# Performance work log

Hardware: AMD Instinct MI355X
Metric: run time of the kernel (lower is better)

Reference implementation:

```python
import jax, jax.numpy as jnp
import numpy as np

B, L1, L2, H = 8, 384, 384, 128


def _lin(k, out_f, in_f, scale=0.05):
    kw, kb = jax.random.split(k)
    return (jax.random.normal(kw, (out_f, in_f), jnp.float32) * scale,
            jax.random.normal(kb, (out_f,), jnp.float32) * scale)


def setup_inputs() -> dict:
    key = jax.random.key(0)
    ks = jax.random.split(key, 10)
    Wq_w, Wq_b = _lin(ks[2], H, H)
    Wup_w, Wup_b = _lin(ks[3], H, H)
    Wvp_w, Wvp_b = _lin(ks[4], H, H)
    V_w, V_b = _lin(ks[5], 1, H)
    Wg_w, Wg_b = _lin(ks[6], 2 * H, 2 * H)
    W_ih, b_ih = _lin(ks[7], 4 * H, 2 * H)
    W_hh, b_hh = _lin(ks[8], 4 * H, H)
    return {
        "x": jax.random.normal(ks[0], (B, L1, H), jnp.float32),
        "x_mask": jnp.zeros((B, L1), dtype=bool),
        "y": jax.random.normal(ks[1], (B, L2, H), jnp.float32),
        "y_mask": jnp.zeros((B, L2), dtype=bool),
        "Wq_w": Wq_w, "Wq_b": Wq_b,
        "Wup_w": Wup_w, "Wup_b": Wup_b,
        "Wvp_w": Wvp_w, "Wvp_b": Wvp_b,
        "V_w": V_w, "V_b": V_b,
        "Wg_w": Wg_w, "Wg_b": Wg_b,
        "W_ih": W_ih, "W_hh": W_hh, "b_ih": b_ih, "b_hh": b_hh,
    }


def reference(x, x_mask, y, y_mask, Wq_w, Wq_b, Wup_w, Wup_b, Wvp_w, Wvp_b,
              V_w, V_b, Wg_w, Wg_b, W_ih, W_hh, b_ih, b_hh):
    b, l1, h = x.shape
    # projections (torch Linear: x @ W.T + b)
    x_proj = x @ Wup_w.T + Wup_b                      # [B, L1, H]
    y_proj = y @ Wq_w.T + Wq_b                        # [B, L2, H]
    # source feeds a constant zero hidden state into W_vp -> just its bias
    hidden_proj = jnp.zeros((h,), x.dtype) @ Wvp_w.T + Wvp_b  # [H]
    # additive attention scores: V . tanh(xp + yp + hp)
    sum_batch = jnp.tanh(x_proj[:, :, None, :] + y_proj[:, None, :, :] + hidden_proj)  # [B,L1,L2,H]
    s = jnp.einsum('btjh,h->btj', sum_batch, V_w[0]) + V_b[0]  # [B, L1, L2]
    # sum_mask = (1 - x_mask) outer (1 - y_mask)
    xm = 1.0 - x_mask.astype(s.dtype)
    ym = 1.0 - y_mask.astype(s.dtype)
    s = s * (xm[:, :, None] * ym[:, None, :])
    s = jnp.where(y_mask[:, None, :], -jnp.inf, s)
    alpha = jax.nn.softmax(s, axis=-1)                # [B, L1, L2]
    ct = jnp.einsum('btj,bjh->bth', alpha, y)         # [B, L1, H]
    merge = jnp.concatenate([x, ct], axis=2)          # [B, L1, 2H]
    gt = jax.nn.sigmoid(merge @ Wg_w.T + Wg_b)
    lstm_in = gt * merge                              # [B, L1, 2H]
    # single-layer unidirectional LSTM (torch gate order: i, f, g, o)
    gates_x = lstm_in @ W_ih.T + b_ih                 # [B, L1, 4H]

    def step(carry, gx):
        h_t, c_t = carry
        g = gx + h_t @ W_hh.T + b_hh
        i, f, gg, o = jnp.split(g, 4, axis=-1)
        c_n = jax.nn.sigmoid(f) * c_t + jax.nn.sigmoid(i) * jnp.tanh(gg)
        h_n = jax.nn.sigmoid(o) * jnp.tanh(c_n)
        return (h_n, c_n), h_n

    init = (jnp.zeros((b, h), x.dtype), jnp.zeros((b, h), x.dtype))
    _, hs = jax.lax.scan(step, init, jnp.swapaxes(gates_x, 0, 1))  # [L1, B, H]
    return jnp.swapaxes(hs, 0, 1)                     # [B, L1, H]
```

## Files before the change

### kernel.cpp

```cpp
#include <hip/hip_runtime.h>
#include <hip/hip_bf16.h>
#include <math.h>

typedef __attribute__((ext_vector_type(4))) float  float4v;
typedef __attribute__((ext_vector_type(2))) float  float2v;
typedef __attribute__((ext_vector_type(8))) short  short8;
typedef __attribute__((ext_vector_type(4))) int    int4v;

#define B_ 8
#define L_ 384
#define H_ 128

__device__ __forceinline__ float bflo(unsigned int u){ unsigned int t = u << 16; float f; __builtin_memcpy(&f,&t,4); return f; }
__device__ __forceinline__ unsigned short f2bf(float f){
  unsigned int t; __builtin_memcpy(&t,&f,4);
  return (unsigned short)((t + 0x7fffu + ((t>>16)&1u)) >> 16);
}
__device__ __forceinline__ float fsig(float x){ return __fdividef(1.f, 1.f + __expf(-x)); }

__device__ __forceinline__ void barrier_lds(){
  asm volatile("s_waitcnt lgkmcnt(0)\n\ts_barrier" ::: "memory");
}

template<int K>
__device__ __forceinline__ void mfma_rowgemm_body(
    unsigned short* in_s,
    const float* __restrict__ inA,
    const float* __restrict__ W, const float* __restrict__ bias,
    const float* __restrict__ bias2, float* __restrict__ out,
    int Ntotal, int act, int row0, int ob)
{
  constexpr int KP = K + 2;
  const int tid  = threadIdx.x;
  const int w    = tid >> 6;
  const int l    = tid & 63;
  const int c    = l & 15;
  const int quad = l >> 4;

  #pragma unroll
  for (int it = 0; it < K/32; ++it) {
    int idx = it*256 + tid;
    int r = idx / (K/4);
    int k = (idx % (K/4)) * 4;
    float4v f = *(const float4v*)(inA + (size_t)(row0+r)*K + k);
    unsigned int p0 = (unsigned int)f2bf(f.x) | ((unsigned int)f2bf(f.y) << 16);
    unsigned int p1 = (unsigned int)f2bf(f.z) | ((unsigned int)f2bf(f.w) << 16);
    *(unsigned int*)&in_s[r*KP + k]     = p0;
    *(unsigned int*)&in_s[r*KP + k + 2] = p1;
  }

  const int n = ob + w*16 + c;
  short8 bfr[K/32];
  #pragma unroll
  for (int kt = 0; kt < K/32; ++kt) {
    const float* src = W + (size_t)n*K + kt*32 + quad*8;
    float4v f0 = *(const float4v*)(src);
    float4v f1 = *(const float4v*)(src + 4);
    short8 v;
    v[0]=(short)f2bf(f0[0]); v[1]=(short)f2bf(f0[1]); v[2]=(short)f2bf(f0[2]); v[3]=(short)f2bf(f0[3]);
    v[4]=(short)f2bf(f1[0]); v[5]=(short)f2bf(f1[1]); v[6]=(short)f2bf(f1[2]); v[7]=(short)f2bf(f1[3]);
    bfr[kt] = v;
  }
  __syncthreads();

  const float4v z4 = {0.f,0.f,0.f,0.f};
  float4v acc0 = z4, acc1 = z4;
  #pragma unroll
  for (int kt = 0; kt < K/32; ++kt) {
    short8 a0 = *(const short8*)&in_s[(c     )*KP + kt*32 + quad*8];
    short8 a1 = *(const short8*)&in_s[(16 + c)*KP + kt*32 + quad*8];
    acc0 = __builtin_amdgcn_mfma_f32_16x16x32_bf16(a0, bfr[kt], acc0, 0,0,0);
    acc1 = __builtin_amdgcn_mfma_f32_16x16x32_bf16(a1, bfr[kt], acc1, 0,0,0);
  }

  const float C2 = 2.8853900817779268f;
  float bv = bias[n] + (bias2 ? bias2[n] : 0.f);
  #pragma unroll
  for (int mt = 0; mt < 2; ++mt) {
    float4v A = mt ? acc1 : acc0;
    #pragma unroll
    for (int r = 0; r < 4; ++r) {
      int m = mt*16 + quad*4 + r;
      float val = A[r] + bv;
      if (act == 4)
        val = __builtin_amdgcn_exp2f(C2 * val);
      if (act == 3)
        out[(size_t)(row0+m)*Ntotal + (n & 127)*4 + (n >> 7)] = val;
      else
        out[(size_t)(row0+m)*Ntotal + n] = val;
    }
  }
}

template<int K>
__global__ __launch_bounds__(256) void mfma_rowgemm_kernel(
    const float* __restrict__ inA,
    const float* __restrict__ W, const float* __restrict__ bias,
    const float* __restrict__ bias2, float* __restrict__ out,
    int Ntotal, int act)
{
  __shared__ __align__(16) unsigned short in_s[32*(K+2)];
  mfma_rowgemm_body<K>(in_s, inA, W, bias, bias2, out,
                       Ntotal, act, blockIdx.x*32, blockIdx.y*64);
}

__global__ __launch_bounds__(256) void proj_mfma_kernel(
    const float* __restrict__ x, const float* __restrict__ y,
    const float* __restrict__ Wup_w, const float* __restrict__ Wup_b,
    const float* __restrict__ Wq_w, const float* __restrict__ Wq_b,
    const float* __restrict__ Wvp_b,
    float* __restrict__ xp, float* __restrict__ yp)
{
  __shared__ __align__(16) unsigned short in_s[32*130];
  int bx = blockIdx.x;
  if (bx < 192)
    mfma_rowgemm_body<128>(in_s, x, Wup_w, Wup_b, nullptr,
                           xp, 128, 4, (bx>>1)*32, (bx&1)*64);
  else {
    bx -= 192;
    mfma_rowgemm_body<128>(in_s, y, Wq_w, Wq_b, Wvp_b,
                           yp, 128, 4, (bx>>1)*32, (bx&1)*64);
  }
}

__global__ __launch_bounds__(256) void attn_kernel(
    const float* __restrict__ xp, const float* __restrict__ yp,
    const float* __restrict__ y, const unsigned char* __restrict__ xmask,
    const unsigned char* __restrict__ ymask, const float* __restrict__ Vw,
    const float* __restrict__ Vb,
    float* __restrict__ ctpbase, float* __restrict__ ml)
{
  __shared__ __align__(16) float xp_s[8][128];
  __shared__ __align__(16) float v2_s[128];
  __shared__ __align__(16) float yp_s[32][132];
  __shared__ __align__(16) unsigned short p_s[16][40];
  __shared__ float sc_s[16];
  __shared__ float xm_s[8];
  __shared__ float ym_s[32];
  __shared__ float sv_s;
  const int tid = threadIdx.x;
  const int b   = blockIdx.y;
  const int t0  = blockIdx.x * 8;
  const int jh  = blockIdx.z;
  const int jb  = jh * 96;
  const int w    = tid >> 6;
  const int l    = tid & 63;
  const int c16  = l & 15;
  const int quad = l >> 4;
  {
    int r = tid >> 5, k4 = (tid & 31) * 4;
    float4v f = *(const float4v*)(xp + ((size_t)(b*L_ + t0 + r))*H_ + k4);
    *(float4v*)&xp_s[r][k4] = f;
    if (tid < 32) {
      float4v v = *(const float4v*)(Vw + tid*4);
      float4v v2; v2[0]=2.f*v[0]; v2[1]=2.f*v[1]; v2[2]=2.f*v[2]; v2[3]=2.f*v[3];
      *(float4v*)&v2_s[tid*4] = v2;
    }
    if (tid < 8) xm_s[tid] = xmask[b*L_ + t0 + tid] ? 0.f : 1.f;
    if (tid < 16) sc_s[tid] = 0.f;
    for (int i = 320 + tid; i < 640; i += 256) ((unsigned short*)p_s)[i] = 0;
  }
  __syncthreads();
  if (tid < 32) {
    float4v v = *(const float4v*)&v2_s[tid*4];
    float sm = (v[0]+v[1]) + (v[2]+v[3]);
    #pragma unroll
    for (int off = 16; off >= 1; off >>= 1) sm += __shfl_xor(sm, off);
    if (tid == 0) sv_s = 0.5f*sm + Vb[0];
  }

  float4v rp[4];
  unsigned char ymb = 0;
  {
    #pragma unroll
    for (int it = 0; it < 4; ++it) {
      int idx = it*256 + tid; int r = idx >> 5; int k4 = (idx & 31) * 4;
      rp[it] = *(const float4v*)(yp + ((size_t)(b*L_ + jb + r))*H_ + k4);
    }
    if (tid < 32) ymb = ymask[b*L_ + jb + tid];
  }

  const int t = tid >> 5, u = tid & 31;
  float mrun = -__builtin_inff(), lrun = 0.f;
  const float4v z4 = {0.f,0.f,0.f,0.f};
  float4v acc0 = z4, acc1 = z4;
  float svc = 0.f, xmv = 0.f;

  for (int c = 0; c < 3; ++c) {
    __syncthreads();
    #pragma unroll
    for (int it = 0; it < 4; ++it) {
      int idx = it*256 + tid; int r = idx >> 5; int k4 = (idx & 31) * 4;
      *(float4v*)&yp_s[r][k4] = rp[it];
    }
    if (tid < 32) ym_s[tid] = ymb ? 0.f : 1.f;
    __syncthreads();
    if (c == 0) { svc = sv_s; xmv = xm_s[t]; }
    short8 yb0, yb1;
    {
      const float* ybase = y + ((size_t)(b*L_ + jb + c*32 + quad*8))*H_ + c16;
      #pragma unroll
      for (int jj = 0; jj < 8; ++jj) {
        yb0[jj] = (short)f2bf(ybase[(size_t)jj*H_ + w*16]);
        yb1[jj] = (short)f2bf(ybase[(size_t)jj*H_ + (w+4)*16]);
      }
    }
    if (c < 2) {
      #pragma unroll
      for (int it = 0; it < 4; ++it) {
        int idx = it*256 + tid; int r = idx >> 5; int k4 = (idx & 31) * 4;
        rp[it] = *(const float4v*)(yp + ((size_t)(b*L_ + jb + (c+1)*32 + r))*H_ + k4);
      }
      if (tid < 32) ymb = ymask[b*L_ + jb + (c+1)*32 + tid];
    }

    float sA = 0.f, sB = 0.f;
    {
      const float* yr = yp_s[u];
      const float* xr = xp_s[t];
      #pragma unroll 4
      for (int k = 0; k < 128; k += 4) {
        float4v yv = *(const float4v*)&yr[k];
        float4v xv = *(const float4v*)&xr[k];
        float4v vv = *(const float4v*)&v2_s[k];
        sA -= vv[0] * __builtin_amdgcn_rcpf(__builtin_fmaf(xv[0], yv[0], 1.f));
        sB -= vv[1] * __builtin_amdgcn_rcpf(__builtin_fmaf(xv[1], yv[1], 1.f));
        sA -= vv[2] * __builtin_amdgcn_rcpf(__builtin_fmaf(xv[2], yv[2], 1.f));
        sB -= vv[3] * __builtin_amdgcn_rcpf(__builtin_fmaf(xv[3], yv[3], 1.f));
      }
    }
    float ymv = ym_s[u];
    float s = (svc + sA + sB) * xmv * ymv;
    if (ymv == 0.f) s = -__builtin_inff();
    float mc = s;
    #pragma unroll
    for (int off = 16; off >= 1; off >>= 1) mc = fmaxf(mc, __shfl_xor(mc, off));
    float mnew = fmaxf(mrun, mc);
    float p  = __expf(s - mnew);
    float sc = __expf(mrun - mnew);
    float ps = p;
    #pragma unroll
    for (int off = 16; off >= 1; off >>= 1) ps += __shfl_xor(ps, off);
    lrun = lrun * sc + ps;
    mrun = mnew;
    p_s[t][u] = f2bf(p);
    if (u == 0) sc_s[t] = sc;
    __syncthreads();
    short8 pf = *(const short8*)&p_s[c16][quad*8];
    float4v scv;
    #pragma unroll
    for (int r = 0; r < 4; ++r) scv[r] = sc_s[quad*4 + r];
    acc0 *= scv; acc1 *= scv;
    acc0 = __builtin_amdgcn_mfma_f32_16x16x32_bf16(pf, yb0, acc0, 0,0,0);
    acc1 = __builtin_amdgcn_mfma_f32_16x16x32_bf16(pf, yb1, acc1, 0,0,0);
  }
  float* ctp = ctpbase + (size_t)jh*393216;
  if (quad < 2) {
    #pragma unroll
    for (int r = 0; r < 4; ++r) {
      int row = b*L_ + t0 + quad*4 + r;
      ctp[(size_t)row*H_ + w*16 + c16]     = acc0[r];
      ctp[(size_t)row*H_ + (w+4)*16 + c16] = acc1[r];
    }
  }
  if (u == 0) {
    int row = b*L_ + t0 + t;
    ml[(jh*2+0)*3072 + row] = mrun;
    ml[(jh*2+1)*3072 + row] = lrun;
  }
}

__global__ __launch_bounds__(256) void gate1_kernel(
    const float* __restrict__ x,
    const float* __restrict__ ctpbase, const float* __restrict__ ml,
    const float* __restrict__ Wg_w, const float* __restrict__ Wg_b,
    float* __restrict__ out)
{
  constexpr int K = 256, KP = 258;
  __shared__ __align__(16) unsigned short in_s[32*KP];
  const int tid  = threadIdx.x;
  const int w    = tid >> 6;
  const int l    = tid & 63;
  const int c    = l & 15;
  const int quad = l >> 4;
  const int row0 = blockIdx.x * 32;
  const int ob   = blockIdx.y * 64;

  #pragma unroll
  for (int it = 0; it < 8; ++it) {
    int idx = it*256 + tid;
    int r = idx >> 6;
    int k = (idx & 63) * 4;
    int row = row0 + r;
    float4v f;
    if (k < 128) {
      f = *(const float4v*)(x + (size_t)row*128 + k);
    } else {
      float m0 = ml[       row], l0 = ml[  3072 + row];
      float m1 = ml[2*3072+row], l1 = ml[3*3072 + row];
      float m2 = ml[4*3072+row], l2 = ml[5*3072 + row];
      float m3 = ml[6*3072+row], l3 = ml[7*3072 + row];
      float mm = fmaxf(fmaxf(m0, m1), fmaxf(m2, m3));
      float e0 = __expf(m0-mm), e1 = __expf(m1-mm);
      float e2 = __expf(m2-mm), e3 = __expf(m3-mm);
      float inv = __fdividef(1.f, (l0*e0 + l1*e1) + (l2*e2 + l3*e3));
      size_t off = (size_t)row*128 + (k-128);
      float4v v0 = *(const float4v*)(ctpbase             + off);
      float4v v1 = *(const float4v*)(ctpbase +   393216  + off);
      float4v v2 = *(const float4v*)(ctpbase + 2*393216  + off);
      float4v v3 = *(const float4v*)(ctpbase + 3*393216  + off);
      f[0] = ((v0[0]*e0 + v1[0]*e1) + (v2[0]*e2 + v3[0]*e3))*inv;
      f[1] = ((v0[1]*e0 + v1[1]*e1) + (v2[1]*e2 + v3[1]*e3))*inv;
      f[2] = ((v0[2]*e0 + v1[2]*e1) + (v2[2]*e2 + v3[2]*e3))*inv;
      f[3] = ((v0[3]*e0 + v1[3]*e1) + (v2[3]*e2 + v3[3]*e3))*inv;
    }
    unsigned int p0 = (unsigned int)f2bf(f[0]) | ((unsigned int)f2bf(f[1]) << 16);
    unsigned int p1 = (unsigned int)f2bf(f[2]) | ((unsigned int)f2bf(f[3]) << 16);
    *(unsigned int*)&in_s[r*KP + k]     = p0;
    *(unsigned int*)&in_s[r*KP + k + 2] = p1;
  }

  const int n = ob + w*16 + c;
  short8 bfr[8];
  #pragma unroll
  for (int kt = 0; kt < 8; ++kt) {
    const float* src = Wg_w + (size_t)n*K + kt*32 + quad*8;
    float4v f0 = *(const float4v*)(src);
    float4v f1 = *(const float4v*)(src + 4);
    short8 v;
    v[0]=(short)f2bf(f0[0]); v[1]=(short)f2bf(f0[1]); v[2]=(short)f2bf(f0[2]); v[3]=(short)f2bf(f0[3]);
    v[4]=(short)f2bf(f1[0]); v[5]=(short)f2bf(f1[1]); v[6]=(short)f2bf(f1[2]); v[7]=(short)f2bf(f1[3]);
    bfr[kt] = v;
  }
  __syncthreads();

  const float4v z4 = {0.f,0.f,0.f,0.f};
  float4v acc0 = z4, acc1 = z4;
  #pragma unroll
  for (int kt = 0; kt < 8; ++kt) {
    short8 a0 = *(const short8*)&in_s[(c     )*KP + kt*32 + quad*8];
    short8 a1 = *(const short8*)&in_s[(16 + c)*KP + kt*32 + quad*8];
    acc0 = __builtin_amdgcn_mfma_f32_16x16x32_bf16(a0, bfr[kt], acc0, 0,0,0);
    acc1 = __builtin_amdgcn_mfma_f32_16x16x32_bf16(a1, bfr[kt], acc1, 0,0,0);
  }

  float bv = Wg_b[n];
  #pragma unroll
  for (int mt = 0; mt < 2; ++mt) {
    float4v A = mt ? acc1 : acc0;
    #pragma unroll
    for (int r = 0; r < 4; ++r) {
      int m = mt*16 + quad*4 + r;
      float val = A[r] + bv;
      float mg = bflo((unsigned int)in_s[m*KP + n]);
      out[(size_t)(row0+m)*256 + n] = fsig(val) * mg;
    }
  }
}

__global__ __launch_bounds__(512) void lstm_kernel(
    const float* __restrict__ gx, const float* __restrict__ Whh,
    float* __restrict__ out)
{
  __shared__ __align__(16) unsigned char h8_s[2][128];
  const int tid  = threadIdx.x;
  const int b    = blockIdx.x;
  const int w    = tid >> 6;
  const int l    = tid & 63;
  const int col  = l & 15;
  const int quad = l >> 4;

  int4v bq[4][2];
  float dq[4];
  #pragma unroll
  for (int nt = 0; nt < 4; ++nt) {
    const int n = nt*128 + w*16 + col;
    const float* src = Whh + (size_t)n*H_;
    float4v f[8];
    #pragma unroll
    for (int t8 = 0; t8 < 2; ++t8)
      #pragma unroll
      for (int i = 0; i < 4; ++i)
        f[t8*4+i] = *(const float4v*)(src + t8*64 + quad*16 + i*4);
    float mx = 0.f;
    #pragma unroll
    for (int i = 0; i < 8; ++i)
      mx = fmaxf(mx, fmaxf(fmaxf(fabsf(f[i][0]), fabsf(f[i][1])),
                           fmaxf(fabsf(f[i][2]), fabsf(f[i][3]))));
    mx = fmaxf(mx, __shfl_xor(mx, 16));
    mx = fmaxf(mx, __shfl_xor(mx, 32));
    const float qs = 127.f / mx;
    dq[nt] = mx * (1.f/16129.f);
    #pragma unroll
    for (int t8 = 0; t8 < 2; ++t8) {
      int4v bb;
      #pragma unroll
      for (int d = 0; d < 4; ++d) {
        float4v ff = f[t8*4+d];
        int q0 = (int)rintf(ff[0]*qs), q1 = (int)rintf(ff[1]*qs);
        int q2 = (int)rintf(ff[2]*qs), q3 = (int)rintf(ff[3]*qs);
        bb[d] = (q0 & 255) | ((q1 & 255) << 8) | ((q2 & 255) << 16) | ((q3 & 255) << 24);
      }
      bq[nt][t8] = bb;
    }
  }

  if (tid < 256) ((unsigned char*)h8_s)[tid] = 0;
  float cst = 0.f;
  const int goff = w*16 + col;
  const float* gbase = gx + (size_t)b*L_*512 + goff*4;
  float* outp = out + (size_t)b*L_*H_ + goff;
  float4v gbuf[4];
  #pragma unroll
  for (int s = 0; s < 4; ++s)
    gbuf[s] = *(const float4v*)(gbase + (size_t)s*512);
  const int4v zi = {0,0,0,0};
  const float NL2E  = -1.4426950408889634f;
  const float P2L2E =  2.8853900817779268f;
  __syncthreads();

  for (int t4 = 0; t4 < L_; t4 += 4) {
    #pragma unroll
    for (int s = 0; s < 4; ++s) {
      const int tstep = t4 + s;
      const unsigned char* hb = h8_s[s & 1];
      int4v a0 = *(const int4v*)&hb[     quad*16];
      int4v a1 = *(const int4v*)&hb[64 + quad*16];
      float4v gcur = gbuf[s];
      if (tstep + 4 < L_)
        gbuf[s] = *(const float4v*)(gbase + (size_t)(tstep+4)*512);
      int4v c0a = __builtin_amdgcn_mfma_i32_16x16x64_i8(a0, bq[0][0], zi, 0,0,0);
      int4v c2a = __builtin_amdgcn_mfma_i32_16x16x64_i8(a0, bq[2][0], zi, 0,0,0);
      int4v c0b = __builtin_amdgcn_mfma_i32_16x16x64_i8(a1, bq[0][1], zi, 0,0,0);
      int4v c2b = __builtin_amdgcn_mfma_i32_16x16x64_i8(a1, bq[2][1], zi, 0,0,0);
      int4v c1a = __builtin_amdgcn_mfma_i32_16x16x64_i8(a0, bq[1][0], zi, 0,0,0);
      int4v c3a = __builtin_amdgcn_mfma_i32_16x16x64_i8(a0, bq[3][0], zi, 0,0,0);
      int4v c1b = __builtin_amdgcn_mfma_i32_16x16x64_i8(a1, bq[1][1], zi, 0,0,0);
      int4v c3b = __builtin_amdgcn_mfma_i32_16x16x64_i8(a1, bq[3][1], zi, 0,0,0);
      float ig = __builtin_amdgcn_rcpf(1.f + __builtin_amdgcn_exp2f(
                   NL2E*__builtin_fmaf((float)(c0a[0]+c0b[0]), dq[0], gcur[0])));
      float gg = 1.f - 2.f*__builtin_amdgcn_rcpf(__builtin_amdgcn_exp2f(
                   P2L2E*__builtin_fmaf((float)(c2a[0]+c2b[0]), dq[2], gcur[2])) + 1.f);
      float igg = ig * gg;
      float fg = __builtin_amdgcn_rcpf(1.f + __builtin_amdgcn_exp2f(
                   NL2E*__builtin_fmaf((float)(c1a[0]+c1b[0]), dq[1], gcur[1])));
      float og = __builtin_amdgcn_rcpf(1.f + __builtin_amdgcn_exp2f(
                   NL2E*__builtin_fmaf((float)(c3a[0]+c3b[0]), dq[3], gcur[3])));
      cst = fg*cst + igg;
      float hn = og * (1.f - 2.f*__builtin_amdgcn_rcpf(
                   __builtin_amdgcn_exp2f(P2L2E*cst) + 1.f));
      if (quad == 0) {
        outp[(size_t)tstep*H_] = hn;
        int q = (int)rintf(hn * 127.f);
        h8_s[(s+1)&1][goff] = (unsigned char)q;
      }
      barrier_lds();
    }
  }
}

extern "C" void kernel_launch(void* const* d_in, const int* in_sizes, int n_in,
                              void* d_out, int out_size, void* d_ws, size_t ws_size,
                              hipStream_t stream)
{
  (void)in_sizes; (void)n_in; (void)out_size; (void)ws_size;
  const float* x     = (const float*)d_in[0];
  const unsigned char* xm = (const unsigned char*)d_in[1];
  const float* y     = (const float*)d_in[2];
  const unsigned char* ym = (const unsigned char*)d_in[3];
  const float* Wq_w  = (const float*)d_in[4];
  const float* Wq_b  = (const float*)d_in[5];
  const float* Wup_w = (const float*)d_in[6];
  const float* Wup_b = (const float*)d_in[7];
  const float* Wvp_b = (const float*)d_in[9];
  const float* V_w   = (const float*)d_in[10];
  const float* V_b   = (const float*)d_in[11];
  const float* Wg_w  = (const float*)d_in[12];
  const float* Wg_b  = (const float*)d_in[13];
  const float* W_ih  = (const float*)d_in[14];
  const float* W_hh  = (const float*)d_in[15];
  const float* b_ih  = (const float*)d_in[16];
  const float* b_hh  = (const float*)d_in[17];
  float* out = (float*)d_out;

  float* wsf    = (float*)d_ws;
  float* xp_ws  = wsf;
  float* yp_ws  = xp_ws + 393216;
  float* li_ws  = xp_ws;
  float* ctp_ws = yp_ws + 393216;
  float* gx_ws  = ctp_ws + 4*393216;
  float* ml_ws  = gx_ws + 1572864;

  proj_mfma_kernel<<<dim3(384),256,0,stream>>>(x, y, Wup_w, Wup_b, Wq_w, Wq_b, Wvp_b, xp_ws, yp_ws);
  attn_kernel<<<dim3(48,8,4),256,0,stream>>>(xp_ws, yp_ws, y, xm, ym, V_w, V_b, ctp_ws, ml_ws);
  gate1_kernel<<<dim3(96,4),256,0,stream>>>(x, ctp_ws, ml_ws, Wg_w, Wg_b, li_ws);
  mfma_rowgemm_kernel<256><<<dim3(96,8),256,0,stream>>>(li_ws, W_ih, b_ih, b_hh, gx_ws, 512, 3);
  lstm_kernel<<<dim3(8),512,0,stream>>>(gx_ws, W_hh, out);
}
```

Baseline: 304.7 us.

## Fuse gate GEMM with LSTM input projection and chain int8 MFMA accumulators

Merges the sigmoid-gate GEMM and the W_ih input-projection GEMM into one kernel. Each block handles 16 rows, keeps the gated merge tile in shared memory as bf16, and streams weight tiles through double-buffered registers, which removes one launch and the intermediate global round trip. In the LSTM step, the two int8 MFMA halves now accumulate into one result instead of being summed afterwards. The trade-off is that every block reloads and converts the full Wg and W_ih weights, and the fused kernel runs on fewer blocks with serialized output tiles.

Measured after the change: 301.0 us. About the same (-1.2%).

```diff
diff --git a/kernel.cpp b/kernel.cpp
--- a/kernel.cpp
+++ b/kernel.cpp
@@ -90,18 +90,6 @@
         out[(size_t)(row0+m)*Ntotal + n] = val;
     }
   }
-}
-
-template<int K>
-__global__ __launch_bounds__(256) void mfma_rowgemm_kernel(
-    const float* __restrict__ inA,
-    const float* __restrict__ W, const float* __restrict__ bias,
-    const float* __restrict__ bias2, float* __restrict__ out,
-    int Ntotal, int act)
-{
-  __shared__ __align__(16) unsigned short in_s[32*(K+2)];
-  mfma_rowgemm_body<K>(in_s, inA, W, bias, bias2, out,
-                       Ntotal, act, blockIdx.x*32, blockIdx.y*64);
 }
 
 __global__ __launch_bounds__(256) void proj_mfma_kernel(
@@ -270,24 +258,26 @@
   }
 }
 
-__global__ __launch_bounds__(256) void gate1_kernel(
+__global__ __launch_bounds__(256) void gatefuse_kernel(
     const float* __restrict__ x,
     const float* __restrict__ ctpbase, const float* __restrict__ ml,
     const float* __restrict__ Wg_w, const float* __restrict__ Wg_b,
-    float* __restrict__ out)
+    const float* __restrict__ Wih, const float* __restrict__ b_ih,
+    const float* __restrict__ b_hh,
+    float* __restrict__ gx)
 {
   constexpr int K = 256, KP = 258;
-  __shared__ __align__(16) unsigned short in_s[32*KP];
+  __shared__ __align__(16) unsigned short in_s[16*KP];
+  __shared__ __align__(16) unsigned short gt_s[16*KP];
   const int tid  = threadIdx.x;
   const int w    = tid >> 6;
   const int l    = tid & 63;
   const int c    = l & 15;
   const int quad = l >> 4;
-  const int row0 = blockIdx.x * 32;
-  const int ob   = blockIdx.y * 64;
-
-  #pragma unroll
-  for (int it = 0; it < 8; ++it) {
+  const int row0 = blockIdx.x * 16;
+
+  #pragma unroll
+  for (int it = 0; it < 4; ++it) {
     int idx = it*256 + tid;
     int r = idx >> 6;
     int k = (idx & 63) * 4;
@@ -320,40 +310,101 @@
     *(unsigned int*)&in_s[r*KP + k + 2] = p1;
   }
 
-  const int n = ob + w*16 + c;
-  short8 bfr[8];
-  #pragma unroll
-  for (int kt = 0; kt < 8; ++kt) {
-    const float* src = Wg_w + (size_t)n*K + kt*32 + quad*8;
-    float4v f0 = *(const float4v*)(src);
-    float4v f1 = *(const float4v*)(src + 4);
-    short8 v;
-    v[0]=(short)f2bf(f0[0]); v[1]=(short)f2bf(f0[1]); v[2]=(short)f2bf(f0[2]); v[3]=(short)f2bf(f0[3]);
-    v[4]=(short)f2bf(f1[0]); v[5]=(short)f2bf(f1[1]); v[6]=(short)f2bf(f1[2]); v[7]=(short)f2bf(f1[3]);
-    bfr[kt] = v;
+  const float4v z4 = {0.f,0.f,0.f,0.f};
+  short8 bfr[2][8];
+
+  {
+    const int n0 = w*16 + c;
+    #pragma unroll
+    for (int kt = 0; kt < 8; ++kt) {
+      const float* src = Wg_w + (size_t)n0*K + kt*32 + quad*8;
+      float4v f0 = *(const float4v*)(src);
+      float4v f1 = *(const float4v*)(src + 4);
+      short8 v;
+      v[0]=(short)f2bf(f0[0]); v[1]=(short)f2bf(f0[1]); v[2]=(short)f2bf(f0[2]); v[3]=(short)f2bf(f0[3]);
+      v[4]=(short)f2bf(f1[0]); v[5]=(short)f2bf(f1[1]); v[6]=(short)f2bf(f1[2]); v[7]=(short)f2bf(f1[3]);
+      bfr[0][kt] = v;
+    }
   }
   __syncthreads();
 
-  const float4v z4 = {0.f,0.f,0.f,0.f};
-  float4v acc0 = z4, acc1 = z4;
-  #pragma unroll
-  for (int kt = 0; kt < 8; ++kt) {
-    short8 a0 = *(const short8*)&in_s[(c     )*KP + kt*32 + quad*8];
-    short8 a1 = *(const short8*)&in_s[(16 + c)*KP + kt*32 + quad*8];
-    acc0 = __builtin_amdgcn_mfma_f32_16x16x32_bf16(a0, bfr[kt], acc0, 0,0,0);
-    acc1 = __builtin_amdgcn_mfma_f32_16x16x32_bf16(a1, bfr[kt], acc1, 0,0,0);
-  }
-
-  float bv = Wg_b[n];
-  #pragma unroll
-  for (int mt = 0; mt < 2; ++mt) {
-    float4v A = mt ? acc1 : acc0;
+  #pragma unroll
+  for (int obi = 0; obi < 4; ++obi) {
+    const int cur = obi & 1;
+    const int n = obi*64 + w*16 + c;
+    if (obi < 3) {
+      const int nn = (obi+1)*64 + w*16 + c;
+      #pragma unroll
+      for (int kt = 0; kt < 8; ++kt) {
+        const float* src = Wg_w + (size_t)nn*K + kt*32 + quad*8;
+        float4v f0 = *(const float4v*)(src);
+        float4v f1 = *(const float4v*)(src + 4);
+        short8 v;
+        v[0]=(short)f2bf(f0[0]); v[1]=(short)f2bf(f0[1]); v[2]=(short)f2bf(f0[2]); v[3]=(short)f2bf(f0[3]);
+        v[4]=(short)f2bf(f1[0]); v[5]=(short)f2bf(f1[1]); v[6]=(short)f2bf(f1[2]); v[7]=(short)f2bf(f1[3]);
+        bfr[cur^1][kt] = v;
+      }
+    }
+    float4v acc0 = z4;
+    #pragma unroll
+    for (int kt = 0; kt < 8; ++kt) {
+      short8 a0 = *(const short8*)&in_s[c*KP + kt*32 + quad*8];
+      acc0 = __builtin_amdgcn_mfma_f32_16x16x32_bf16(a0, bfr[cur][kt], acc0, 0,0,0);
+    }
+    float bv = Wg_b[n];
     #pragma unroll
     for (int r = 0; r < 4; ++r) {
-      int m = mt*16 + quad*4 + r;
-      float val = A[r] + bv;
+      int m = quad*4 + r;
+      float val = acc0[r] + bv;
       float mg = bflo((unsigned int)in_s[m*KP + n]);
-      out[(size_t)(row0+m)*256 + n] = fsig(val) * mg;
+      gt_s[m*KP + n] = f2bf(fsig(val) * mg);
+    }
+  }
+
+  {
+    const int n0 = w*16 + c;
+    #pragma unroll
+    for (int kt = 0; kt < 8; ++kt) {
+      const float* src = Wih + (size_t)n0*K + kt*32 + quad*8;
+      float4v f0 = *(const float4v*)(src);
+      float4v f1 = *(const float4v*)(src + 4);
+      short8 v;
+      v[0]=(short)f2bf(f0[0]); v[1]=(short)f2bf(f0[1]); v[2]=(short)f2bf(f0[2]); v[3]=(short)f2bf(f0[3]);
+      v[4]=(short)f2bf(f1[0]); v[5]=(short)f2bf(f1[1]); v[6]=(short)f2bf(f1[2]); v[7]=(short)f2bf(f1[3]);
+      bfr[0][kt] = v;
+    }
+  }
+  __syncthreads();
+
+  #pragma unroll
+  for (int oby = 0; oby < 8; ++oby) {
+    const int cur = oby & 1;
+    const int n = oby*64 + w*16 + c;
+    if (oby < 7) {
+      const int nn = (oby+1)*64 + w*16 + c;
+      #pragma unroll
+      for (int kt = 0; kt < 8; ++kt) {
+        const float* src = Wih + (size_t)nn*K + kt*32 + quad*8;
+        float4v f0 = *(const float4v*)(src);
+        float4v f1 = *(const float4v*)(src + 4);
+        short8 v;
+        v[0]=(short)f2bf(f0[0]); v[1]=(short)f2bf(f0[1]); v[2]=(short)f2bf(f0[2]); v[3]=(short)f2bf(f0[3]);
+        v[4]=(short)f2bf(f1[0]); v[5]=(short)f2bf(f1[1]); v[6]=(short)f2bf(f1[2]); v[7]=(short)f2bf(f1[3]);
+        bfr[cur^1][kt] = v;
+      }
+    }
+    float4v acc0 = z4;
+    #pragma unroll
+    for (int kt = 0; kt < 8; ++kt) {
+      short8 a0 = *(const short8*)&gt_s[c*KP + kt*32 + quad*8];
+      acc0 = __builtin_amdgcn_mfma_f32_16x16x32_bf16(a0, bfr[cur][kt], acc0, 0,0,0);
+    }
+    float bv = b_ih[n] + b_hh[n];
+    #pragma unroll
+    for (int r = 0; r < 4; ++r) {
+      int m = quad*4 + r;
+      float val = acc0[r] + bv;
+      gx[(size_t)(row0+m)*512 + (n & 127)*4 + (n >> 7)] = val;
     }
   }
 }
@@ -429,23 +480,23 @@
       float4v gcur = gbuf[s];
       if (tstep + 4 < L_)
         gbuf[s] = *(const float4v*)(gbase + (size_t)(tstep+4)*512);
-      int4v c0a = __builtin_amdgcn_mfma_i32_16x16x64_i8(a0, bq[0][0], zi, 0,0,0);
-      int4v c2a = __builtin_amdgcn_mfma_i32_16x16x64_i8(a0, bq[2][0], zi, 0,0,0);
-      int4v c0b = __builtin_amdgcn_mfma_i32_16x16x64_i8(a1, bq[0][1], zi, 0,0,0);
-      int4v c2b = __builtin_amdgcn_mfma_i32_16x16x64_i8(a1, bq[2][1], zi, 0,0,0);
-      int4v c1a = __builtin_amdgcn_mfma_i32_16x16x64_i8(a0, bq[1][0], zi, 0,0,0);
-      int4v c3a = __builtin_amdgcn_mfma_i32_16x16x64_i8(a0, bq[3][0], zi, 0,0,0);
-      int4v c1b = __builtin_amdgcn_mfma_i32_16x16x64_i8(a1, bq[1][1], zi, 0,0,0);
-      int4v c3b = __builtin_amdgcn_mfma_i32_16x16x64_i8(a1, bq[3][1], zi, 0,0,0);
+      int4v c0 = __builtin_amdgcn_mfma_i32_16x16x64_i8(a0, bq[0][0], zi, 0,0,0);
+      int4v c2 = __builtin_amdgcn_mfma_i32_16x16x64_i8(a0, bq[2][0], zi, 0,0,0);
+      c0 = __builtin_amdgcn_mfma_i32_16x16x64_i8(a1, bq[0][1], c0, 0,0,0);
+      c2 = __builtin_amdgcn_mfma_i32_16x16x64_i8(a1, bq[2][1], c2, 0,0,0);
+      int4v c1 = __builtin_amdgcn_mfma_i32_16x16x64_i8(a0, bq[1][0], zi, 0,0,0);
+      int4v c3 = __builtin_amdgcn_mfma_i32_16x16x64_i8(a0, bq[3][0], zi, 0,0,0);
+      c1 = __builtin_amdgcn_mfma_i32_16x16x64_i8(a1, bq[1][1], c1, 0,0,0);
+      c3 = __builtin_amdgcn_mfma_i32_16x16x64_i8(a1, bq[3][1], c3, 0,0,0);
       float ig = __builtin_amdgcn_rcpf(1.f + __builtin_amdgcn_exp2f(
-                   NL2E*__builtin_fmaf((float)(c0a[0]+c0b[0]), dq[0], gcur[0])));
+                   NL2E*__builtin_fmaf((float)c0[0], dq[0], gcur[0])));
       float gg = 1.f - 2.f*__builtin_amdgcn_rcpf(__builtin_amdgcn_exp2f(
-                   P2L2E*__builtin_fmaf((float)(c2a[0]+c2b[0]), dq[2], gcur[2])) + 1.f);
+                   P2L2E*__builtin_fmaf((float)c2[0], dq[2], gcur[2])) + 1.f);
       float igg = ig * gg;
       float fg = __builtin_amdgcn_rcpf(1.f + __builtin_amdgcn_exp2f(
-                   NL2E*__builtin_fmaf((float)(c1a[0]+c1b[0]), dq[1], gcur[1])));
+                   NL2E*__builtin_fmaf((float)c1[0], dq[1], gcur[1])));
       float og = __builtin_amdgcn_rcpf(1.f + __builtin_amdgcn_exp2f(
-                   NL2E*__builtin_fmaf((float)(c3a[0]+c3b[0]), dq[3], gcur[3])));
+                   NL2E*__builtin_fmaf((float)c3[0], dq[3], gcur[3])));
       cst = fg*cst + igg;
       float hn = og * (1.f - 2.f*__builtin_amdgcn_rcpf(
                    __builtin_amdgcn_exp2f(P2L2E*cst) + 1.f));
@@ -486,14 +537,12 @@
   float* wsf    = (float*)d_ws;
   float* xp_ws  = wsf;
   float* yp_ws  = xp_ws + 393216;
-  float* li_ws  = xp_ws;
   float* ctp_ws = yp_ws + 393216;
   float* gx_ws  = ctp_ws + 4*393216;
   float* ml_ws  = gx_ws + 1572864;
 
   proj_mfma_kernel<<<dim3(384),256,0,stream>>>(x, y, Wup_w, Wup_b, Wq_w, Wq_b, Wvp_b, xp_ws, yp_ws);
   attn_kernel<<<dim3(48,8,4),256,0,stream>>>(xp_ws, yp_ws, y, xm, ym, V_w, V_b, ctp_ws, ml_ws);
-  gate1_kernel<<<dim3(96,4),256,0,stream>>>(x, ctp_ws, ml_ws, Wg_w, Wg_b, li_ws);
-  mfma_rowgemm_kernel<256><<<dim3(96,8),256,0,stream>>>(li_ws, W_ih, b_ih, b_hh, gx_ws, 512, 3);
+  gatefuse_kernel<<<dim3(192),256,0,stream>>>(x, ctp_ws, ml_ws, Wg_w, Wg_b, W_ih, b_ih, b_hh, gx_ws);
   lstm_kernel<<<dim3(8),512,0,stream>>>(gx_ws, W_hh, out);
 }
```
